# Kernel tuning notes

Measured on AMD Instinct MI355X. Metric: run time of the kernel, lower is better.

Reference implementation:

```python
import jax, jax.numpy as jnp
import numpy as np

K = 3  # deformable kernel size -> K*K = 9 sampling points
EPS = 1e-5


def _bilinear_sample(img, py, px):
    """Bilinear sample img (B,H,W,C) at float pixel coords py,px (B,H,W), zero padding."""
    B, H, W, C = img.shape
    y0f = jnp.floor(py); x0f = jnp.floor(px)
    wy = py - y0f; wx = px - x0f
    y0 = y0f.astype(jnp.int32); x0 = x0f.astype(jnp.int32)
    bidx = jnp.arange(B)[:, None, None]
    out = jnp.zeros(img.shape, img.dtype)
    corners = ((0, 0, (1 - wy) * (1 - wx)), (0, 1, (1 - wy) * wx),
               (1, 0, wy * (1 - wx)), (1, 1, wy * wx))
    for dy, dx, w in corners:
        yy = y0 + dy; xx = x0 + dx
        valid = ((yy >= 0) & (yy < H) & (xx >= 0) & (xx < W)).astype(img.dtype)
        yc = jnp.clip(yy, 0, H - 1); xc = jnp.clip(xx, 0, W - 1)
        out = out + (w * valid)[..., None] * img[bidx, yc, xc]
    return out


def setup_inputs() -> dict:
    key = jax.random.key(0)
    ks = jax.random.split(key, 8)
    B, C, H, W = 8, 256, 64, 64
    return {
        "x1": jax.random.normal(ks[0], (B, C, H, W), jnp.float32),
        "x2": jax.random.normal(ks[1], (B, C, H // 2, W // 2), jnp.float32),
        "dw_w": jax.random.normal(ks[2], (3, 3, 1, C), jnp.float32) * 0.05,
        "dw_b": jnp.zeros((C,), jnp.float32),
        "ln_g": jnp.ones((C,), jnp.float32),
        "ln_b": jnp.zeros((C,), jnp.float32),
        "off_w": jax.random.normal(ks[3], (C, 2 * K * K), jnp.float32) * 0.01,
        "off_b": jnp.zeros((2 * K * K,), jnp.float32),
        "mask_w": jax.random.normal(ks[4], (C, K * K), jnp.float32) * 0.02,
        "mask_b": jnp.zeros((K * K,), jnp.float32),
        "in_w": jax.random.normal(ks[5], (C, C), jnp.float32) * 0.02,
        "in_b": jnp.zeros((C,), jnp.float32),
        "out_w": jax.random.normal(ks[6], (C, C), jnp.float32) * 0.02,
        "out_b": jnp.zeros((C,), jnp.float32),
        "bn_g": jnp.ones((C,), jnp.float32),
        "bn_b": jnp.zeros((C,), jnp.float32),
        "bn_mean": jnp.zeros((C,), jnp.float32),
        "bn_var": jnp.ones((C,), jnp.float32),
    }


def _forward(x1, x2, dw_w, dw_b, ln_g, ln_b, off_w, off_b, mask_w, mask_b,
             in_w, in_b, out_w, out_b, bn_g, bn_b, bn_mean, bn_var):
    B, C, H, W = x1.shape
    # interpolate x2 -> (H,W), bilinear (half-pixel centers, align_corners=False)
    x2r = jax.image.resize(x2, (B, C, H, W), method="linear")
    x21, x22 = jnp.split(x2r, 2, axis=0)
    diff = jnp.abs(x21 - x22)
    guide = jnp.concatenate([diff, diff], axis=0)  # repeat(2,1,1,1)

    v = jnp.transpose(x1, (0, 2, 3, 1))      # (B,H,W,C) values
    f = jnp.transpose(guide, (0, 2, 3, 1))   # (B,H,W,C) guidance

    # DCNv3 input projection
    x_proj = v @ in_w + in_b

    # depthwise 3x3 conv + LayerNorm + GELU on guidance
    feat = jax.lax.conv_general_dilated(
        f, dw_w, (1, 1), "SAME",
        dimension_numbers=("NHWC", "HWIO", "NHWC"),
        feature_group_count=C) + dw_b
    mu = jnp.mean(feat, axis=-1, keepdims=True)
    var = jnp.var(feat, axis=-1, keepdims=True)
    feat = (feat - mu) * jax.lax.rsqrt(var + EPS) * ln_g + ln_b
    feat = jax.nn.gelu(feat)

    offset = (feat @ off_w + off_b).reshape(B, H, W, K * K, 2)  # (..., (dx,dy))
    mask = jax.nn.softmax(feat @ mask_w + mask_b, axis=-1)       # (B,H,W,9)

    base_y = jnp.arange(H, dtype=x1.dtype)[:, None]
    base_x = jnp.arange(W, dtype=x1.dtype)[None, :]
    acc = jnp.zeros((B, H, W, C), x1.dtype)
    for k in range(K * K):
        ky = k // K - 1
        kx = k % K - 1
        py = base_y + ky + offset[..., k, 1]
        px = base_x + kx + offset[..., k, 0]
        acc = acc + mask[..., k:k + 1] * _bilinear_sample(x_proj, py, px)

    y = acc @ out_w + out_b                  # output projection
    y = jnp.transpose(y, (0, 3, 1, 2))       # back to NCHW

    # BatchNorm (inference stats) + ReLU + residual
    scale = bn_g * jax.lax.rsqrt(bn_var + EPS)
    y = y * scale[None, :, None, None] + (bn_b - bn_mean * scale)[None, :, None, None]
    return jax.nn.relu(y) + x1


def reference(x1, x2, dw_w, dw_b, ln_g, ln_b, off_w, off_b, mask_w, mask_b,
              in_w, in_b, out_w, out_b, bn_g, bn_b, bn_mean, bn_var):
    return _forward(x1, x2, dw_w, dw_b, ln_g, ln_b, off_w, off_b, mask_w, mask_b,
                    in_w, in_b, out_w, out_b, bn_g, bn_b, bn_mean, bn_var)
```

## Files before the change

### kernel.cpp

```cpp
#include <hip/hip_runtime.h>
#include <math.h>

#define BB 8
#define CC 256
#define HH 64
#define WW 64
#define H2 32
#define W2 32
#define NPIX (BB*HH*WW)
#define EPSV 1e-5f

typedef unsigned short ushortT;
using short8  = __attribute__((ext_vector_type(8))) short;
using floatx4 = __attribute__((ext_vector_type(4))) float;

__device__ inline float b2f(ushortT u) {
    unsigned int x = ((unsigned int)u) << 16;
    float f; __builtin_memcpy(&f, &x, 4); return f;
}
__device__ inline ushortT f2b(float f) {
    unsigned int x; __builtin_memcpy(&x, &f, 4);
    unsigned int r = x + 0x7fffu + ((x >> 16) & 1u);
    return (ushortT)(r >> 16);
}

__global__ __launch_bounds__(256) void k1_both(const float* __restrict__ x2,
        const float* __restrict__ x1, const float* __restrict__ in_w,
        const float* __restrict__ in_b, const float* __restrict__ out_w,
        const float* __restrict__ off_w, const float* __restrict__ mask_w,
        ushortT* __restrict__ guide, ushortT* __restrict__ x1t,
        ushortT* __restrict__ Bf, float* __restrict__ bwout,
        ushortT* __restrict__ Whf) {
    __shared__ __align__(16) char smem[21248];
    int blk0 = blockIdx.x;
    int t = threadIdx.x;

    if (blk0 >= 6401) {
        int s = (blk0 - 6401) * 256 + t;
        int lane = s & 63;
        int kt = (s >> 6) & 7;
        int nt = s >> 9;
        int n = nt * 16 + (lane & 15);
        int k = kt * 32 + (lane >> 4) * 8;
        short8 o;
        #pragma unroll
        for (int j = 0; j < 8; ++j) {
            float wv = 0.f;
            int kk = k + j;
            if (n < 18)      wv = off_w[kk * 18 + n];
            else if (n < 27) wv = mask_w[kk * 9 + (n - 18)];
            o[j] = (short)f2b(wv);
        }
        *(short8*)(Whf + (size_t)s * 8) = o;
        return;
    }
    if (blk0 >= 6144) {
        float* Wl = (float*)smem;
        int j = blk0 - 6144;
        int n = t;
        Wl[n] = (j < CC) ? in_w[(size_t)j * CC + n] : in_b[n];
        __syncthreads();
        float acc = 0.f;
        #pragma unroll 8
        for (int k = 0; k < CC; ++k)
            acc = fmaf(Wl[k], out_w[(size_t)k * CC + n], acc);
        if (j < CC) {
            int lane = (((j >> 3) & 3) << 4) | (n & 15);
            size_t idx = ((size_t)(((n >> 4) * 8 + (j >> 5)) * 64 + lane)) * 8 + (j & 7);
            Bf[idx] = f2b(acc);
        } else {
            bwout[n] = acc;
        }
        return;
    }

    if (blk0 < 4096) {
        float*   Xs   = (float*)smem;
        ushortT* tile = (ushortT*)(smem + 16896);
        int c0 = (blk0 & 7) * 32;
        int y  = (blk0 >> 3) & 63;
        int b  = blk0 >> 9;
        int bb = b & 3;
        float sy = 0.5f * y - 0.25f;
        float fy0 = floorf(sy);
        float wy = sy - fy0;
        int jy0 = (int)fy0;
        int iy0 = max(0, min(H2 - 1, jy0));
        int iy1 = max(0, min(H2 - 1, jy0 + 1));
        #pragma unroll
        for (int i = 0; i < 4; ++i) {
            int e = t + i * 256;
            int q = e >> 9, ch = (e >> 4) & 31, r = (e >> 3) & 1, xg = (e & 7) * 4;
            int iy = r ? iy1 : iy0;
            float4 v = *(const float4*)(x2 +
                (size_t)(((bb + 4 * q) * CC + c0 + ch) * H2 + iy) * W2 + xg);
            float* dst = Xs + (size_t)((q * 32 + ch) * 2 + r) * 33 + xg;
            dst[0] = v.x; dst[1] = v.y; dst[2] = v.z; dst[3] = v.w;
        }
        __syncthreads();
        int x = t & 63, cl = t >> 6;
        float sx = 0.5f * x - 0.25f;
        float fx0 = floorf(sx);
        float wx = sx - fx0;
        int jx0 = (int)fx0;
        int ix0 = max(0, min(W2 - 1, jx0));
        int ix1 = max(0, min(W2 - 1, jx0 + 1));
        float w00 = (1.f - wy) * (1.f - wx), w01 = (1.f - wy) * wx;
        float w10 = wy * (1.f - wx), w11 = wy * wx;
        #pragma unroll
        for (int it = 0; it < 8; ++it) {
            int c = cl + it * 4;
            const float* a  = Xs + (size_t)(c * 2) * 33;
            const float* bq = Xs + (size_t)((32 + c) * 2) * 33;
            float v1 = w00 * a[ix0]  + w01 * a[ix1]  + w10 * a[33 + ix0]  + w11 * a[33 + ix1];
            float v2 = w00 * bq[ix0] + w01 * bq[ix1] + w10 * bq[33 + ix0] + w11 * bq[33 + ix1];
            tile[x * 34 + c] = f2b(fabsf(v1 - v2));
        }
        __syncthreads();
        {
            int px = t >> 2, oct = t & 3;
            uint4 o;
            o.x = *(const unsigned int*)(&tile[px * 34 + oct * 8 + 0]);
            o.y = *(const unsigned int*)(&tile[px * 34 + oct * 8 + 2]);
            o.z = *(const unsigned int*)(&tile[px * 34 + oct * 8 + 4]);
            o.w = *(const unsigned int*)(&tile[px * 34 + oct * 8 + 6]);
            *(uint4*)(guide + (size_t)((b * HH + y) * WW + px) * CC + c0 + oct * 8) = o;
        }
    } else {
        ushortT* tile = (ushortT*)smem;
        int blk = blk0 - 4096;
        int c0 = (blk & 3) * 64;
        int y  = (blk >> 2) & 63;
        int b  = blk >> 8;
        #pragma unroll
        for (int i = 0; i < 4; ++i) {
            int e = t + i * 256;
            int ch = e >> 4, xq = (e & 15) * 4;
            float4 v = *(const float4*)(x1 + (size_t)((b * CC + c0 + ch) * HH + y) * WW + xq);
            tile[(xq + 0) * 66 + ch] = f2b(v.x);
            tile[(xq + 1) * 66 + ch] = f2b(v.y);
            tile[(xq + 2) * 66 + ch] = f2b(v.z);
            tile[(xq + 3) * 66 + ch] = f2b(v.w);
        }
        __syncthreads();
        #pragma unroll
        for (int i = 0; i < 2; ++i) {
            int e = t + i * 256;
            int px = e >> 3, oct = e & 7;
            uint4 o;
            o.x = *(const unsigned int*)(&tile[px * 66 + oct * 8 + 0]);
            o.y = *(const unsigned int*)(&tile[px * 66 + oct * 8 + 2]);
            o.z = *(const unsigned int*)(&tile[px * 66 + oct * 8 + 4]);
            o.w = *(const unsigned int*)(&tile[px * 66 + oct * 8 + 6]);
            *(uint4*)(x1t + (size_t)((b * HH + y) * WW + px) * CC + c0 + oct * 8) = o;
        }
    }
}

__global__ __launch_bounds__(512, 4) void k2ab(const ushortT* __restrict__ guide,
        const float* __restrict__ dw_w, const float* __restrict__ dw_b,
        const float* __restrict__ ln_g, const float* __restrict__ ln_b,
        const ushortT* __restrict__ Whf, const float* __restrict__ off_b,
        const float* __restrict__ mask_b, float* __restrict__ offmask) {
    __shared__ __align__(16) short sfeat[32 * 264];
    __shared__ float O[32 * 36];
    int t = threadIdx.x;
    int blk = ((blockIdx.x & 7) << 7) | (blockIdx.x >> 3);
    int b = blk >> 7, y = (blk >> 1) & 63, xh = (blk & 1) * 32;
    int lane = t & 63, w = t >> 6;
    int cl = lane & 15, rg = lane >> 4;

    {
        int pxl = t >> 4, s = t & 15;
        int c0 = s * 16;
        int xg = xh + pxl;
        float f[16];
        #pragma unroll
        for (int q = 0; q < 4; ++q) {
            float4 d = *(const float4*)(dw_b + c0 + q * 4);
            f[q*4+0]=d.x; f[q*4+1]=d.y; f[q*4+2]=d.z; f[q*4+3]=d.w;
        }
        #pragma unroll
        for (int tap = 0; tap < 9; ++tap) {
            int dy = tap / 3 - 1, dxx = tap % 3 - 1;
            int yy = y + dy, xx = xg + dxx;
            if (yy >= 0 && yy < HH && xx >= 0 && xx < WW) {
                const ushortT* gp = guide + (size_t)((b * HH + yy) * WW + xx) * CC + c0;
                #pragma unroll
                for (int q = 0; q < 2; ++q) {
                    short8 v = *(const short8*)(gp + q * 8);
                    float4 w0 = *(const float4*)(dw_w + tap * CC + c0 + q * 8);
                    float4 w1 = *(const float4*)(dw_w + tap * CC + c0 + q * 8 + 4);
                    float wv[8] = {w0.x, w0.y, w0.z, w0.w, w1.x, w1.y, w1.z, w1.w};
                    #pragma unroll
                    for (int j2 = 0; j2 < 8; ++j2)
                        f[q*8 + j2] = fmaf(b2f((ushortT)v[j2]), wv[j2], f[q*8 + j2]);
                }
            }
        }
        float s1 = 0.f, s2 = 0.f;
        #pragma unroll
        for (int j = 0; j < 16; ++j) { s1 += f[j]; s2 += f[j] * f[j]; }
        #pragma unroll
        for (int off = 8; off; off >>= 1) {
            s1 += __shfl_xor(s1, off);
            s2 += __shfl_xor(s2, off);
        }
        float mean = s1 * (1.0f / CC);
        float var  = s2 * (1.0f / CC) - mean * mean;
        float rs = rsqrtf(var + EPSV);
        #pragma unroll
        for (int q = 0; q < 2; ++q) {
            float4 g0 = *(const float4*)(ln_g + c0 + q * 8);
            float4 g1 = *(const float4*)(ln_g + c0 + q * 8 + 4);
            float4 e0 = *(const float4*)(ln_b + c0 + q * 8);
            float4 e1 = *(const float4*)(ln_b + c0 + q * 8 + 4);
            float gv[8] = {g0.x, g0.y, g0.z, g0.w, g1.x, g1.y, g1.z, g1.w};
            float ev[8] = {e0.x, e0.y, e0.z, e0.w, e1.x, e1.y, e1.z, e1.w};
            short8 sv;
            #pragma unroll
            for (int j2 = 0; j2 < 8; ++j2) {
                float v = (f[q*8 + j2] - mean) * rs * gv[j2] + ev[j2];
                float u2 = 1.5957691216057308f * (v + 0.044715f * v * v * v);
                v = v * __frcp_rn(1.0f + __expf(-u2));
                sv[j2] = (short)f2b(v);
            }
            *(short8*)(&sfeat[pxl * 264 + c0 + q * 8]) = sv;
        }
    }
    __syncthreads();

    if (w < 4) {
        int mt = w >> 1, nt = w & 1;
        floatx4 acc = {0.f, 0.f, 0.f, 0.f};
        #pragma unroll
        for (int kt = 0; kt < 8; ++kt) {
            short8 af  = *(const short8*)(&sfeat[(mt * 16 + cl) * 264 + kt * 32 + rg * 8]);
            short8 bf2 = *(const short8*)(Whf + ((size_t)((nt * 8 + kt) * 64 + lane)) * 8);
            acc = __builtin_amdgcn_mfma_f32_16x16x32_bf16(af, bf2, acc, 0, 0, 0);
        }
        int col = nt * 16 + cl;
        float bias = (col < 18) ? off_b[col] : ((col < 27) ? mask_b[col - 18] : 0.f);
        #pragma unroll
        for (int j = 0; j < 4; ++j) {
            int row = mt * 16 + rg * 4 + j;
            O[row * 36 + col] = acc[j] + bias;
        }
    }
    __syncthreads();

    if (t < 32) {
        float* row = O + t * 36 + 18;
        float mx = row[0];
        #pragma unroll
        for (int k = 1; k < 9; ++k) mx = fmaxf(mx, row[k]);
        float e9[9], ssum = 0.f;
        #pragma unroll
        for (int k = 0; k < 9; ++k) { e9[k] = __expf(row[k] - mx); ssum += e9[k]; }
        float inv = __frcp_rn(ssum);
        #pragma unroll
        for (int k = 0; k < 9; ++k) row[k] = e9[k] * inv;
    }
    __syncthreads();
    #pragma unroll
    for (int i = 0; i < 2; ++i) {
        int idx = t + i * 512;
        int p = idx >> 5, jj = idx & 31;
        offmask[((size_t)blk * 32 + p) * 32 + jj] = O[p * 36 + jj];
    }
}

#define GATHER_CHUNK(K0) do {                                            \
        int c_ = (K0) + o8 * 8;                                          \
        _Pragma("unroll")                                                \
        for (int q = 0; q < 36; ++q) {                                   \
            float wv_ = wp[q];                                           \
            short8 v_ = *(const short8*)(x1t + ip[q] + c_);              \
            _Pragma("unroll")                                            \
            for (int j = 0; j < 8; ++j)                                  \
                f[j] = fmaf(wv_, b2f((ushortT)v_[j]), f[j]);             \
        }                                                                \
    } while (0)

__global__ __launch_bounds__(512, 4) void k45_fused(const ushortT* __restrict__ x1t,
        const float* __restrict__ offmask, const ushortT* __restrict__ Bf,
        const float* __restrict__ bwout, const float* __restrict__ out_b,
        const float* __restrict__ bn_g, const float* __restrict__ bn_b,
        const float* __restrict__ bn_mean, const float* __restrict__ bn_var,
        const float* __restrict__ x1, float* __restrict__ out) {
    __shared__ __align__(16) char smem[40192];
    short* Asb     = (short*)smem;
    float* s_w     = (float*)(smem + 18432);
    int*   s_idx   = (int*)(smem + 27648);
    float* s_scale = (float*)(smem + 36864);
    float* s_shift = (float*)(smem + 37888);
    float* s_bw    = (float*)(smem + 38912);
    float* s_sum   = (float*)(smem + 39936);
    float* Lo      = (float*)smem;

    int t = threadIdx.x;
    int bm = ((blockIdx.x & 7) << 6) | (blockIdx.x >> 3);
    int m0 = bm * 64;
    int b = bm >> 6, y = bm & 63;
    int lane = t & 63, w = t >> 6;
    int cl = lane & 15, rg = lane >> 4;

    if (t < 256) {
        float scale = bn_g[t] * rsqrtf(bn_var[t] + EPSV);
        s_scale[t] = scale;
        s_shift[t] = out_b[t] * scale + bn_b[t] - bn_mean[t] * scale;
        s_bw[t]    = bwout[t] * scale;
    }
    for (int e = t; e < 576; e += 512) {
        int px = e / 9, k = e - px * 9;
        int p = m0 + px;
        float dxo = offmask[(size_t)p * 32 + 2 * k];
        float dyo = offmask[(size_t)p * 32 + 2 * k + 1];
        float mk  = offmask[(size_t)p * 32 + 18 + k];
        float py  = (float)y  + (float)(k / 3 - 1) + dyo;
        float pxf = (float)px + (float)(k % 3 - 1) + dxo;
        float y0f = floorf(py), x0f = floorf(pxf);
        float wy = py - y0f, wx = pxf - x0f;
        int y0 = (int)y0f, x0 = (int)x0f;
        int y1 = y0 + 1, x1i = x0 + 1;
        float vy0 = (y0 >= 0 && y0 < HH) ? 1.f : 0.f;
        float vy1 = (y1 >= 0 && y1 < HH) ? 1.f : 0.f;
        float vx0 = (x0 >= 0 && x0 < WW) ? 1.f : 0.f;
        float vx1 = (x1i >= 0 && x1i < WW) ? 1.f : 0.f;
        int yc0 = max(0, min(HH - 1, y0)), yc1 = max(0, min(HH - 1, y1));
        int xc0 = max(0, min(WW - 1, x0)), xc1 = max(0, min(WW - 1, x1i));
        int base = b * HH * WW;
        int o = (px * 9 + k) * 4;
        s_idx[o + 0] = (base + yc0 * WW + xc0) * CC;
        s_idx[o + 1] = (base + yc0 * WW + xc1) * CC;
        s_idx[o + 2] = (base + yc1 * WW + xc0) * CC;
        s_idx[o + 3] = (base + yc1 * WW + xc1) * CC;
        s_w[o + 0] = mk * (1.f - wy) * (1.f - wx) * vy0 * vx0;
        s_w[o + 1] = mk * (1.f - wy) * wx * vy0 * vx1;
        s_w[o + 2] = mk * wy * (1.f - wx) * vy1 * vx0;
        s_w[o + 3] = mk * wy * wx * vy1 * vx1;
    }
    __syncthreads();
    if (t < 64) {
        float s = 0.f;
        #pragma unroll
        for (int q = 0; q < 36; ++q) s += s_w[t * 36 + q];
        s_sum[t] = s;
    }
    __syncthreads();

    int px = t >> 3, o8 = t & 7;
    const float* wp = s_w  + px * 36;
    const int*   ip = s_idx + px * 36;

    floatx4 acc[4][2];
    floatx4 zero = {0.f, 0.f, 0.f, 0.f};
    #pragma unroll
    for (int i = 0; i < 4; ++i)
        #pragma unroll
        for (int j = 0; j < 2; ++j) acc[i][j] = zero;

    {
        float f[8] = {};
        GATHER_CHUNK(0);
        short8 sv;
        #pragma unroll
        for (int j = 0; j < 8; ++j) sv[j] = (short)f2b(f[j]);
        *(short8*)(&Asb[px * 72 + o8 * 8]) = sv;
    }
    __syncthreads();

    #pragma unroll
    for (int kc = 0; kc < 4; ++kc) {
        int cur = kc & 1;
        float f[8] = {};
        if (kc < 3)
            GATHER_CHUNK((kc + 1) * 64);
        {
            const short* Ab = Asb + cur * 4608;
            int kt0 = kc * 2;
            #pragma unroll
            for (int kk = 0; kk < 2; ++kk) {
                short8 af[4], bfr[2];
                #pragma unroll
                for (int fr2 = 0; fr2 < 4; ++fr2)
                    af[fr2] = *(const short8*)(&Ab[(fr2 * 16 + cl) * 72 + kk * 32 + rg * 8]);
                #pragma unroll
                for (int fc = 0; fc < 2; ++fc)
                    bfr[fc] = *(const short8*)(Bf + ((size_t)((w * 2 + fc) * 8 + kt0 + kk) * 64 + lane) * 8);
                #pragma unroll
                for (int fr2 = 0; fr2 < 4; ++fr2)
                    #pragma unroll
                    for (int fc = 0; fc < 2; ++fc)
                        acc[fr2][fc] = __builtin_amdgcn_mfma_f32_16x16x32_bf16(
                            af[fr2], bfr[fc], acc[fr2][fc], 0, 0, 0);
            }
        }
        if (kc < 3) {
            short8 sv;
            #pragma unroll
            for (int j = 0; j < 8; ++j) sv[j] = (short)f2b(f[j]);
            *(short8*)(&Asb[(cur ^ 1) * 4608 + px * 72 + o8 * 8]) = sv;
        }
        __syncthreads();
    }

    #pragma unroll
    for (int ph = 0; ph < 4; ++ph) {
        if ((w >> 1) == ph) {
            #pragma unroll
            for (int fc = 0; fc < 2; ++fc) {
                int cloc = (w & 1) * 32 + fc * 16 + cl;
                #pragma unroll
                for (int fr2 = 0; fr2 < 4; ++fr2) {
                    int mr = fr2 * 16 + rg * 4;
                    #pragma unroll
                    for (int j = 0; j < 4; ++j)
                        Lo[(mr + j) * 65 + cloc] = acc[fr2][fc][j];
                }
            }
        }
        __syncthreads();
        #pragma unroll
        for (int i = 0; i < 8; ++i) {
            int e = t + i * 512;
            int xl = e & 63, cw = e >> 6;
            int co = ph * 64 + cw;
            float val = Lo[xl * 65 + cw] * s_scale[co] + s_sum[xl] * s_bw[co] + s_shift[co];
            val = fmaxf(val, 0.f);
            size_t g = (size_t)((b * CC + co) * HH + y) * WW + xl;
            out[g] = val + x1[g];
        }
        __syncthreads();
    }
}

extern "C" void kernel_launch(void* const* d_in, const int* in_sizes, int n_in,
                              void* d_out, int out_size, void* d_ws, size_t ws_size,
                              hipStream_t stream) {
    const float* x1     = (const float*)d_in[0];
    const float* x2     = (const float*)d_in[1];
    const float* dw_w   = (const float*)d_in[2];
    const float* dw_b   = (const float*)d_in[3];
    const float* ln_g   = (const float*)d_in[4];
    const float* ln_b   = (const float*)d_in[5];
    const float* off_w  = (const float*)d_in[6];
    const float* off_b  = (const float*)d_in[7];
    const float* mask_w = (const float*)d_in[8];
    const float* mask_b = (const float*)d_in[9];
    const float* in_w   = (const float*)d_in[10];
    const float* in_b   = (const float*)d_in[11];
    const float* out_w  = (const float*)d_in[12];
    const float* out_b  = (const float*)d_in[13];
    const float* bn_g   = (const float*)d_in[14];
    const float* bn_b   = (const float*)d_in[15];
    const float* bn_mean= (const float*)d_in[16];
    const float* bn_var = (const float*)d_in[17];
    float* out = (float*)d_out;

    char* wsb = (char*)d_ws;
    const size_t SZ = (size_t)NPIX * CC * 2;
    ushortT* guide   = (ushortT*)wsb;
    ushortT* x1t     = (ushortT*)(wsb + SZ);
    float*   offmask = (float*)(wsb + 2 * SZ);
    float*   bwout   = offmask + (size_t)NPIX * 32;
    ushortT* Bf      = (ushortT*)(bwout + CC);
    ushortT* Whf     = Bf + (size_t)CC * CC;

    hipLaunchKernelGGL(k1_both, dim3(6405), dim3(256), 0, stream, x2, x1, in_w, in_b,
                       out_w, off_w, mask_w, guide, x1t, Bf, bwout, Whf);
    hipLaunchKernelGGL(k2ab,    dim3(1024), dim3(512), 0, stream, guide, dw_w, dw_b,
                       ln_g, ln_b, Whf, off_b, mask_b, offmask);
    hipLaunchKernelGGL(k45_fused, dim3(512), dim3(512), 0, stream, x1t, offmask, Bf,
                       bwout, out_b, bn_g, bn_b, bn_mean, bn_var, x1, out);
}
```

Measured before the change: 95.73 us.

## Stage five-row input window in LDS for deformable gather when offsets stay local

When every sampled row for a block falls within y±2, the kernel copies a 5-row by 64-pixel by 64-channel slab of the bf16 input into shared memory for each channel chunk. The 36 bilinear taps are then read from LDS instead of issuing scattered global loads, and the gather indices are rewritten into slab offsets. If any offset leaves that window it falls back to the old global gather. The old double-buffered overlap of gather with MFMA is dropped, and LDS use grows to about 72KB, which lowers occupancy and adds a sync per chunk.

```diff
diff --git a/kernel.cpp b/kernel.cpp
--- a/kernel.cpp
+++ b/kernel.cpp
@@ -270,32 +270,21 @@
     }
 }
 
-#define GATHER_CHUNK(K0) do {                                            \
-        int c_ = (K0) + o8 * 8;                                          \
-        _Pragma("unroll")                                                \
-        for (int q = 0; q < 36; ++q) {                                   \
-            float wv_ = wp[q];                                           \
-            short8 v_ = *(const short8*)(x1t + ip[q] + c_);              \
-            _Pragma("unroll")                                            \
-            for (int j = 0; j < 8; ++j)                                  \
-                f[j] = fmaf(wv_, b2f((ushortT)v_[j]), f[j]);             \
-        }                                                                \
-    } while (0)
-
 __global__ __launch_bounds__(512, 4) void k45_fused(const ushortT* __restrict__ x1t,
         const float* __restrict__ offmask, const ushortT* __restrict__ Bf,
         const float* __restrict__ bwout, const float* __restrict__ out_b,
         const float* __restrict__ bn_g, const float* __restrict__ bn_b,
         const float* __restrict__ bn_mean, const float* __restrict__ bn_var,
         const float* __restrict__ x1, float* __restrict__ out) {
-    __shared__ __align__(16) char smem[40192];
-    short* Asb     = (short*)smem;
-    float* s_w     = (float*)(smem + 18432);
-    int*   s_idx   = (int*)(smem + 27648);
-    float* s_scale = (float*)(smem + 36864);
-    float* s_shift = (float*)(smem + 37888);
-    float* s_bw    = (float*)(smem + 38912);
-    float* s_sum   = (float*)(smem + 39936);
+    __shared__ __align__(16) char smem[71936];
+    short* stg     = (short*)smem;
+    short* Asb     = (short*)(smem + 40960);
+    float* s_w     = (float*)(smem + 50176);
+    int*   s_idx   = (int*)(smem + 59392);
+    float* s_scale = (float*)(smem + 68608);
+    float* s_shift = (float*)(smem + 69632);
+    float* s_bw    = (float*)(smem + 70656);
+    float* s_sum   = (float*)(smem + 71680);
     float* Lo      = (float*)smem;
 
     int t = threadIdx.x;
@@ -304,6 +293,8 @@
     int b = bm >> 6, y = bm & 63;
     int lane = t & 63, w = t >> 6;
     int cl = lane & 15, rg = lane >> 4;
+    int rbase = max(0, y - 2);
+    int rtop  = min(HH - 1, y + 2);
 
     if (t < 256) {
         float scale = bn_g[t] * rsqrtf(bn_var[t] + EPSV);
@@ -311,6 +302,7 @@
         s_shift[t] = out_b[t] * scale + bn_b[t] - bn_mean[t] * scale;
         s_bw[t]    = bwout[t] * scale;
     }
+    int ok = 1;
     for (int e = t; e < 576; e += 512) {
         int px = e / 9, k = e - px * 9;
         int p = m0 + px;
@@ -329,6 +321,7 @@
         float vx1 = (x1i >= 0 && x1i < WW) ? 1.f : 0.f;
         int yc0 = max(0, min(HH - 1, y0)), yc1 = max(0, min(HH - 1, y1));
         int xc0 = max(0, min(WW - 1, x0)), xc1 = max(0, min(WW - 1, x1i));
+        ok &= (yc0 >= rbase && yc0 <= rtop && yc1 >= rbase && yc1 <= rtop) ? 1 : 0;
         int base = b * HH * WW;
         int o = (px * 9 + k) * 4;
         s_idx[o + 0] = (base + yc0 * WW + xc0) * CC;
@@ -340,12 +333,16 @@
         s_w[o + 2] = mk * wy * (1.f - wx) * vy1 * vx0;
         s_w[o + 3] = mk * wy * wx * vy1 * vx1;
     }
-    __syncthreads();
+    int allok = __syncthreads_and(ok);
     if (t < 64) {
         float s = 0.f;
         #pragma unroll
         for (int q = 0; q < 36; ++q) s += s_w[t * 36 + q];
         s_sum[t] = s;
+    }
+    if (allok) {
+        for (int e = t; e < 2304; e += 512)
+            s_idx[e] = (((s_idx[e] >> 8) - b * (HH * WW)) - rbase * WW) << 6;
     }
     __syncthreads();
 
@@ -360,47 +357,61 @@
         #pragma unroll
         for (int j = 0; j < 2; ++j) acc[i][j] = zero;
 
-    {
-        float f[8] = {};
-        GATHER_CHUNK(0);
-        short8 sv;
-        #pragma unroll
-        for (int j = 0; j < 8; ++j) sv[j] = (short)f2b(f[j]);
-        *(short8*)(&Asb[px * 72 + o8 * 8]) = sv;
-    }
-    __syncthreads();
-
-    #pragma unroll
-    for (int kc = 0; kc < 4; ++kc) {
-        int cur = kc & 1;
-        float f[8] = {};
-        if (kc < 3)
-            GATHER_CHUNK((kc + 1) * 64);
-        {
-            const short* Ab = Asb + cur * 4608;
-            int kt0 = kc * 2;
-            #pragma unroll
-            for (int kk = 0; kk < 2; ++kk) {
-                short8 af[4], bfr[2];
+    for (int k0 = 0; k0 < CC; k0 += 64) {
+        if (allok) {
+            #pragma unroll
+            for (int li = 0; li < 5; ++li) {
+                int row = min(HH - 1, rbase + li);
+                *(short8*)(&stg[(li * 64 + px) * 64 + o8 * 8]) =
+                    *(const short8*)(x1t + ((size_t)(b * (HH * WW) + row * WW + px)) * CC + k0 + o8 * 8);
+            }
+            __syncthreads();
+            float f[8] = {};
+            #pragma unroll
+            for (int q = 0; q < 36; ++q) {
+                float wv = wp[q];
+                short8 v = *(const short8*)(&stg[ip[q] + o8 * 8]);
                 #pragma unroll
-                for (int fr2 = 0; fr2 < 4; ++fr2)
-                    af[fr2] = *(const short8*)(&Ab[(fr2 * 16 + cl) * 72 + kk * 32 + rg * 8]);
+                for (int j = 0; j < 8; ++j)
+                    f[j] = fmaf(wv, b2f((ushortT)v[j]), f[j]);
+            }
+            short8 sv;
+            #pragma unroll
+            for (int j = 0; j < 8; ++j) sv[j] = (short)f2b(f[j]);
+            *(short8*)(&Asb[px * 72 + o8 * 8]) = sv;
+        } else {
+            int c = k0 + o8 * 8;
+            float f[8] = {};
+            #pragma unroll
+            for (int q = 0; q < 36; ++q) {
+                float wv = wp[q];
+                short8 v = *(const short8*)(x1t + ip[q] + c);
+                #pragma unroll
+                for (int j = 0; j < 8; ++j)
+                    f[j] = fmaf(wv, b2f((ushortT)v[j]), f[j]);
+            }
+            short8 sv;
+            #pragma unroll
+            for (int j = 0; j < 8; ++j) sv[j] = (short)f2b(f[j]);
+            *(short8*)(&Asb[px * 72 + o8 * 8]) = sv;
+        }
+        __syncthreads();
+        int kt0 = k0 >> 5;
+        #pragma unroll
+        for (int kk = 0; kk < 2; ++kk) {
+            short8 af[4], bfr[2];
+            #pragma unroll
+            for (int f2 = 0; f2 < 4; ++f2)
+                af[f2] = *(const short8*)(&Asb[(f2 * 16 + cl) * 72 + kk * 32 + rg * 8]);
+            #pragma unroll
+            for (int fc = 0; fc < 2; ++fc)
+                bfr[fc] = *(const short8*)(Bf + ((size_t)((w * 2 + fc) * 8 + kt0 + kk) * 64 + lane) * 8);
+            #pragma unroll
+            for (int fr = 0; fr < 4; ++fr)
                 #pragma unroll
                 for (int fc = 0; fc < 2; ++fc)
-                    bfr[fc] = *(const short8*)(Bf + ((size_t)((w * 2 + fc) * 8 + kt0 + kk) * 64 + lane) * 8);
-                #pragma unroll
-                for (int fr2 = 0; fr2 < 4; ++fr2)
-                    #pragma unroll
-                    for (int fc = 0; fc < 2; ++fc)
-                        acc[fr2][fc] = __builtin_amdgcn_mfma_f32_16x16x32_bf16(
-                            af[fr2], bfr[fc], acc[fr2][fc], 0, 0, 0);
-            }
-        }
-        if (kc < 3) {
-            short8 sv;
-            #pragma unroll
-            for (int j = 0; j < 8; ++j) sv[j] = (short)f2b(f[j]);
-            *(short8*)(&Asb[(cur ^ 1) * 4608 + px * 72 + o8 * 8]) = sv;
+                    acc[fr][fc] = __builtin_amdgcn_mfma_f32_16x16x32_bf16(
+                        af[fr], bfr[fc], acc[fr][fc], 0, 0, 0);
         }
         __syncthreads();
     }
@@ -412,11 +423,11 @@
             for (int fc = 0; fc < 2; ++fc) {
                 int cloc = (w & 1) * 32 + fc * 16 + cl;
                 #pragma unroll
-                for (int fr2 = 0; fr2 < 4; ++fr2) {
-                    int mr = fr2 * 16 + rg * 4;
+                for (int fr = 0; fr < 4; ++fr) {
+                    int mr = fr * 16 + rg * 4;
                     #pragma unroll
                     for (int j = 0; j < 4; ++j)
-                        Lo[(mr + j) * 65 + cloc] = acc[fr2][fc][j];
+                        Lo[(mr + j) * 65 + cloc] = acc[fr][fc][j];
                 }
             }
         }
```

After: 98.38 us. 1.03x slower.
